# Kernel tuning notes

Hardware: AMD Instinct MI355X
Metric: run time of the kernel (lower is better)

Reference implementation:

```python
import jax, jax.numpy as jnp
import numpy as np

SEQ, B, D_IN, H = 2048, 64, 256, 256


def setup_inputs() -> dict:
    key = jax.random.key(0)
    k1, k2, k3, k4, k5 = jax.random.split(key, 5)
    stdv = 1.0 / np.sqrt(H)
    return {
        "x": jax.random.normal(k1, (SEQ, B, D_IN), dtype=jnp.float32),
        "w_ih": jax.random.uniform(k2, (H, D_IN), dtype=jnp.float32, minval=-stdv, maxval=stdv),
        "w_hh": jax.random.uniform(k3, (H, H), dtype=jnp.float32, minval=-stdv, maxval=stdv),
        "b_ih": jax.random.uniform(k4, (H,), dtype=jnp.float32, minval=-stdv, maxval=stdv),
        "b_hh": jax.random.uniform(k5, (H,), dtype=jnp.float32, minval=-stdv, maxval=stdv),
    }


def reference(x, w_ih, w_hh, b_ih, b_hh):
    # x: [T, B, D_in]. Precompute the input projection + biases for all steps
    # (this part is parallel across time); the recurrence runs via lax.scan.
    xw = jnp.einsum('tbi,hi->tbh', x, w_ih) + b_ih + b_hh  # [T, B, H]
    w_hh_t = w_hh.T

    def step(h, xt):
        h_new = jnp.tanh(xt + h @ w_hh_t)
        return h_new, h_new

    h0 = jnp.zeros((x.shape[1], w_hh.shape[0]), dtype=x.dtype)
    _, hs = jax.lax.scan(step, h0, xw)
    return hs  # [T, B, H], seq-major (batch_first=False)
```

## Files before the change

kernel.cpp:

```cpp
#include <hip/hip_runtime.h>
#include <cstdint>
#include <cstddef>

#define T_SEQ 2048
#define BATCH 64
#define DIN   256
#define HDIM  256

typedef float    f32x4 __attribute__((ext_vector_type(4)));
typedef short    s16x8 __attribute__((ext_vector_type(8)));
typedef uint32_t u32x2 __attribute__((ext_vector_type(2)));

__device__ inline uint32_t cvt_pk_bf16(float lo, float hi) {
  uint32_t r;
  asm("v_cvt_pk_bf16_f32 %0, %1, %2" : "=v"(r) : "v"(lo), "v"(hi));
  return r;
}

__device__ inline float fast_tanh(float x) {
  float s = x * 2.885390081777927f;
  float e2, r;
  asm("v_exp_f32 %0, %1" : "=v"(e2) : "v"(s));
  float d = 1.0f + e2;
  asm("v_rcp_f32 %0, %1" : "=v"(r) : "v"(d));
  return __builtin_fmaf(-2.0f, r, 1.0f);
}

__global__ __launch_bounds__(256, 2) void rnn_xproj(
    const float* __restrict__ x, const float* __restrict__ w_ih,
    const float* __restrict__ b_ih, const float* __restrict__ b_hh,
    float* __restrict__ out)
{
  __shared__ __align__(16) unsigned short xtile[64 * 264];
  const int tid  = threadIdx.x;
  const int wv   = tid >> 6;
  const int lane = tid & 63;
  const int q    = lane >> 4;
  const int r16  = lane & 15;
  const int m0   = blockIdx.x * 64;

  s16x8 afr[4][8];
#pragma unroll
  for (int nn = 0; nn < 4; ++nn) {
    const int j = 64 * wv + 16 * nn + r16;
#pragma unroll
    for (int kk = 0; kk < 8; ++kk) {
      const int k0 = kk * 32 + q * 8;
      f32x4 lo = *(const f32x4*)(w_ih + j * DIN + k0);
      f32x4 hi = *(const f32x4*)(w_ih + j * DIN + k0 + 4);
      union { s16x8 v; uint32_t u[4]; } fu;
      fu.u[0] = cvt_pk_bf16(lo.x, lo.y);
      fu.u[1] = cvt_pk_bf16(lo.z, lo.w);
      fu.u[2] = cvt_pk_bf16(hi.x, hi.y);
      fu.u[3] = cvt_pk_bf16(hi.z, hi.w);
      afr[nn][kk] = fu.v;
    }
  }

  f32x4 bs[4];
#pragma unroll
  for (int nn = 0; nn < 4; ++nn) {
    const int j0 = 64 * wv + 16 * nn + 4 * q;
    f32x4 a = *(const f32x4*)(b_ih + j0);
    f32x4 b = *(const f32x4*)(b_hh + j0);
    bs[nn] = a + b;
  }

#pragma unroll
  for (int s = 0; s < 16; ++s) {
    const int o   = s * 1024 + tid * 4;
    const int row = o >> 8;
    const int col = o & 255;
    f32x4 v = *(const f32x4*)(x + (size_t)m0 * DIN + o);
    u32x2 pk;
    pk.x = cvt_pk_bf16(v.x, v.y);
    pk.y = cvt_pk_bf16(v.z, v.w);
    *(u32x2*)((char*)xtile + row * 528 + col * 2) = pk;
  }
  __syncthreads();

#pragma unroll
  for (int mm = 0; mm < 4; ++mm) {
    s16x8 bfr[8];
#pragma unroll
    for (int kk = 0; kk < 8; ++kk)
      bfr[kk] = *(const s16x8*)((const char*)xtile +
                                (16 * mm + r16) * 528 + kk * 64 + q * 16);
#pragma unroll
    for (int nn = 0; nn < 4; ++nn) {
      f32x4 acc = {0.f, 0.f, 0.f, 0.f};
#pragma unroll
      for (int kk = 0; kk < 8; ++kk)
        acc = __builtin_amdgcn_mfma_f32_16x16x32_bf16(afr[nn][kk], bfr[kk], acc, 0, 0, 0);
      const int m  = m0 + 16 * mm + r16;
      const int j0 = 64 * wv + 16 * nn + 4 * q;
      f32x4 v = acc + bs[nn];
      *(f32x4*)(out + (size_t)m * HDIM + j0) = v;
    }
  }
}

__global__ __launch_bounds__(256, 1) void rnn_recur(
    const float* __restrict__ w_hh, float* out)
{
  __shared__ __align__(16) unsigned short hbuf[2 * 16 * 264];
  const int tid  = threadIdx.x;
  const int wv   = tid >> 6;
  const int lane = tid & 63;
  const int q    = lane >> 4;
  const int r16  = lane & 15;
  const int g    = blockIdx.x;

  s16x8 afr[4][8];
#pragma unroll
  for (int nn = 0; nn < 4; ++nn) {
    const int j = 64 * wv + 16 * nn + r16;
#pragma unroll
    for (int kk = 0; kk < 8; ++kk) {
      const int k0 = kk * 32 + q * 8;
      f32x4 lo = *(const f32x4*)(w_hh + j * HDIM + k0);
      f32x4 hi = *(const f32x4*)(w_hh + j * HDIM + k0 + 4);
      union { s16x8 v; uint32_t u[4]; } fu;
      fu.u[0] = cvt_pk_bf16(lo.x, lo.y);
      fu.u[1] = cvt_pk_bf16(lo.z, lo.w);
      fu.u[2] = cvt_pk_bf16(hi.x, hi.y);
      fu.u[3] = cvt_pk_bf16(hi.z, hi.w);
      afr[nn][kk] = fu.v;
    }
  }

  for (int i = tid; i < 2 * 16 * 264; i += 256) hbuf[i] = 0;

  const int brow = (16 * g + r16) * HDIM;
  __syncthreads();

  f32x4 xw_cur[4];
#pragma unroll
  for (int nn = 0; nn < 4; ++nn)
    xw_cur[nn] = *(const f32x4*)(out + brow + 64 * wv + 16 * nn + 4 * q);

  int p = 0;
  for (int t = 0; t < T_SEQ; ++t) {
    const size_t tn = (size_t)((t + 1 < T_SEQ) ? (t + 1) : 0) * (BATCH * HDIM);
    f32x4 xw_nxt[4];
#pragma unroll
    for (int nn = 0; nn < 4; ++nn)
      xw_nxt[nn] = *(const f32x4*)(out + tn + brow + 64 * wv + 16 * nn + 4 * q);

    const char* hb = (const char*)hbuf + p * (16 * 264 * 2);
    s16x8 bfr[8];
#pragma unroll
    for (int kk = 0; kk < 8; ++kk)
      bfr[kk] = *(const s16x8*)(hb + r16 * 528 + kk * 64 + q * 16);

    char* hw = (char*)hbuf + (p ^ 1) * (16 * 264 * 2);
    const size_t tc = (size_t)t * (BATCH * HDIM);
#pragma unroll
    for (int nn = 0; nn < 4; ++nn) {
      f32x4 acc = {0.f, 0.f, 0.f, 0.f};
#pragma unroll
      for (int kk = 0; kk < 8; ++kk)
        acc = __builtin_amdgcn_mfma_f32_16x16x32_bf16(afr[nn][kk], bfr[kk], acc, 0, 0, 0);
      const int j0 = 64 * wv + 16 * nn + 4 * q;
      f32x4 v;
      v.x = fast_tanh(acc.x + xw_cur[nn].x);
      v.y = fast_tanh(acc.y + xw_cur[nn].y);
      v.z = fast_tanh(acc.z + xw_cur[nn].z);
      v.w = fast_tanh(acc.w + xw_cur[nn].w);
      *(f32x4*)(out + tc + brow + j0) = v;
      u32x2 pk;
      pk.x = cvt_pk_bf16(v.x, v.y);
      pk.y = cvt_pk_bf16(v.z, v.w);
      *(u32x2*)(hw + r16 * 528 + j0 * 2) = pk;
    }
    __syncthreads();
#pragma unroll
    for (int nn = 0; nn < 4; ++nn) xw_cur[nn] = xw_nxt[nn];
    p ^= 1;
  }
}

extern "C" void kernel_launch(void* const* d_in, const int* in_sizes, int n_in,
                              void* d_out, int out_size, void* d_ws, size_t ws_size,
                              hipStream_t stream) {
  (void)in_sizes; (void)n_in; (void)d_ws; (void)ws_size; (void)out_size;
  const float* x    = (const float*)d_in[0];
  const float* w_ih = (const float*)d_in[1];
  const float* w_hh = (const float*)d_in[2];
  const float* b_ih = (const float*)d_in[3];
  const float* b_hh = (const float*)d_in[4];
  float* out = (float*)d_out;

  rnn_xproj<<<dim3(131072 / 64), dim3(256), 0, stream>>>(x, w_ih, b_ih, b_hh, out);
  rnn_recur<<<dim3(4), dim3(256), 0, stream>>>(w_hh, out);
}
```

Before: 2.452 ms.

## Split recurrence over 8 blocks of 512 threads with 8 batch rows each

New measurement: 2.232 ms. 1.1x faster.

```diff
diff --git a/kernel.cpp b/kernel.cpp
--- a/kernel.cpp
+++ b/kernel.cpp
@@ -26,7 +26,7 @@
   return __builtin_fmaf(-2.0f, r, 1.0f);
 }
 
-__global__ __launch_bounds__(256, 2) void rnn_xproj(
+__global__ __launch_bounds__(256) void rnn_xproj(
     const float* __restrict__ x, const float* __restrict__ w_ih,
     const float* __restrict__ b_ih, const float* __restrict__ b_hh,
     float* __restrict__ out)
@@ -100,7 +100,7 @@
   }
 }
 
-__global__ __launch_bounds__(256, 1) void rnn_recur(
+__global__ __launch_bounds__(512, 2) void rnn_recur(
     const float* __restrict__ w_hh, float* out)
 {
   __shared__ __align__(16) unsigned short hbuf[2 * 16 * 264];
@@ -109,12 +109,13 @@
   const int lane = tid & 63;
   const int q    = lane >> 4;
   const int r16  = lane & 15;
+  const int r8   = r16 & 7;
   const int g    = blockIdx.x;
 
-  s16x8 afr[4][8];
-#pragma unroll
-  for (int nn = 0; nn < 4; ++nn) {
-    const int j = 64 * wv + 16 * nn + r16;
+  s16x8 afr[2][8];
+#pragma unroll
+  for (int nn = 0; nn < 2; ++nn) {
+    const int j = 32 * wv + 16 * nn + r16;
 #pragma unroll
     for (int kk = 0; kk < 8; ++kk) {
       const int k0 = kk * 32 + q * 8;
@@ -129,53 +130,72 @@
     }
   }
 
-  for (int i = tid; i < 2 * 16 * 264; i += 256) hbuf[i] = 0;
-
-  const int brow = (16 * g + r16) * HDIM;
+  for (int i = tid; i < 2 * 16 * 264; i += 512) hbuf[i] = 0;
   __syncthreads();
 
-  f32x4 xw_cur[4];
-#pragma unroll
-  for (int nn = 0; nn < 4; ++nn)
-    xw_cur[nn] = *(const f32x4*)(out + brow + 64 * wv + 16 * nn + 4 * q);
+  const int browL = (8 * g + r8)  * HDIM;
+  const int browS = (8 * g + r16) * HDIM;
+  const int jA = 32 * wv + 4 * q;
+  const int jB = jA + 16;
+  const size_t STEP = (size_t)BATCH * HDIM;
+
+  f32x4 xwA_c = *(const f32x4*)(out + browL + jA);
+  f32x4 xwB_c = *(const f32x4*)(out + browL + jB);
+  f32x4 xwA_n = *(const f32x4*)(out + STEP + browL + jA);
+  f32x4 xwB_n = *(const f32x4*)(out + STEP + browL + jB);
 
   int p = 0;
   for (int t = 0; t < T_SEQ; ++t) {
-    const size_t tn = (size_t)((t + 1 < T_SEQ) ? (t + 1) : 0) * (BATCH * HDIM);
-    f32x4 xw_nxt[4];
-#pragma unroll
-    for (int nn = 0; nn < 4; ++nn)
-      xw_nxt[nn] = *(const f32x4*)(out + tn + brow + 64 * wv + 16 * nn + 4 * q);
+    const int tf = (t + 2 < T_SEQ) ? (t + 2) : (t + 2 - T_SEQ);
+    const size_t fo = (size_t)tf * STEP + browL;
+    f32x4 xwA_f = *(const f32x4*)(out + fo + jA);
+    f32x4 xwB_f = *(const f32x4*)(out + fo + jB);
 
     const char* hb = (const char*)hbuf + p * (16 * 264 * 2);
     s16x8 bfr[8];
 #pragma unroll
     for (int kk = 0; kk < 8; ++kk)
-      bfr[kk] = *(const s16x8*)(hb + r16 * 528 + kk * 64 + q * 16);
+      bfr[kk] = *(const s16x8*)(hb + r8 * 528 + kk * 64 + q * 16);
 
     char* hw = (char*)hbuf + (p ^ 1) * (16 * 264 * 2);
-    const size_t tc = (size_t)t * (BATCH * HDIM);
-#pragma unroll
-    for (int nn = 0; nn < 4; ++nn) {
-      f32x4 acc = {0.f, 0.f, 0.f, 0.f};
-#pragma unroll
-      for (int kk = 0; kk < 8; ++kk)
-        acc = __builtin_amdgcn_mfma_f32_16x16x32_bf16(afr[nn][kk], bfr[kk], acc, 0, 0, 0);
-      const int j0 = 64 * wv + 16 * nn + 4 * q;
-      f32x4 v;
-      v.x = fast_tanh(acc.x + xw_cur[nn].x);
-      v.y = fast_tanh(acc.y + xw_cur[nn].y);
-      v.z = fast_tanh(acc.z + xw_cur[nn].z);
-      v.w = fast_tanh(acc.w + xw_cur[nn].w);
-      *(f32x4*)(out + tc + brow + j0) = v;
-      u32x2 pk;
-      pk.x = cvt_pk_bf16(v.x, v.y);
-      pk.y = cvt_pk_bf16(v.z, v.w);
-      *(u32x2*)(hw + r16 * 528 + j0 * 2) = pk;
-    }
-    __syncthreads();
-#pragma unroll
-    for (int nn = 0; nn < 4; ++nn) xw_cur[nn] = xw_nxt[nn];
+    const size_t tc = (size_t)t * STEP;
+
+    f32x4 accA = {0.f, 0.f, 0.f, 0.f};
+    f32x4 accB = {0.f, 0.f, 0.f, 0.f};
+#pragma unroll
+    for (int kk = 0; kk < 8; ++kk) {
+      accA = __builtin_amdgcn_mfma_f32_16x16x32_bf16(afr[0][kk], bfr[kk], accA, 0, 0, 0);
+      accB = __builtin_amdgcn_mfma_f32_16x16x32_bf16(afr[1][kk], bfr[kk], accB, 0, 0, 0);
+    }
+
+    f32x4 vA, vB;
+    vA.x = fast_tanh(accA.x + xwA_c.x);
+    vA.y = fast_tanh(accA.y + xwA_c.y);
+    vA.z = fast_tanh(accA.z + xwA_c.z);
+    vA.w = fast_tanh(accA.w + xwA_c.w);
+    vB.x = fast_tanh(accB.x + xwB_c.x);
+    vB.y = fast_tanh(accB.y + xwB_c.y);
+    vB.z = fast_tanh(accB.z + xwB_c.z);
+    vB.w = fast_tanh(accB.w + xwB_c.w);
+
+    if (r16 < 8) {
+      *(f32x4*)(out + tc + browS + jA) = vA;
+      *(f32x4*)(out + tc + browS + jB) = vB;
+      u32x2 pkA, pkB;
+      pkA.x = cvt_pk_bf16(vA.x, vA.y);
+      pkA.y = cvt_pk_bf16(vA.z, vA.w);
+      pkB.x = cvt_pk_bf16(vB.x, vB.y);
+      pkB.y = cvt_pk_bf16(vB.z, vB.w);
+      *(u32x2*)(hw + r16 * 528 + jA * 2) = pkA;
+      *(u32x2*)(hw + r16 * 528 + jB * 2) = pkB;
+    }
+
+    asm volatile("s_waitcnt lgkmcnt(0)" ::: "memory");
+    __builtin_amdgcn_s_barrier();
+    __builtin_amdgcn_sched_barrier(0);
+
+    xwA_c = xwA_n; xwB_c = xwB_n;
+    xwA_n = xwA_f; xwB_n = xwB_f;
     p ^= 1;
   }
 }
@@ -192,5 +212,5 @@
   float* out = (float*)d_out;
 
   rnn_xproj<<<dim3(131072 / 64), dim3(256), 0, stream>>>(x, w_ih, b_ih, b_hh, out);
-  rnn_recur<<<dim3(4), dim3(256), 0, stream>>>(w_hh, out);
-}
+  rnn_recur<<<dim3(8), dim3(512), 0, stream>>>(w_hh, out);
+}
```
